# Performance work log

Measured on AMD Instinct MI355X. Metric: run time of the kernel, lower is better.

## Reference

```python
import jax, jax.numpy as jnp
import numpy as np

N, E = 50000, 800000
NFEAT, NHID, NCLASS = 512, 256, 64
RRELU_SLOPE = (1.0 / 8.0 + 1.0 / 3.0) / 2.0  # nn.RReLU eval-mode negative slope


def spmm(row, col, val, X):
    # sparse adj (COO: row, col, val) @ dense X -> [N, F]
    return jax.ops.segment_sum(X[col] * val[:, None], row, num_segments=N)


def setup_inputs() -> dict:
    key = jax.random.key(0)
    ks = jax.random.split(key, 12)
    x = jax.random.normal(ks[0], (N, NFEAT), dtype=jnp.float32)
    edge_row = jnp.sort(jax.random.randint(ks[1], (E,), 0, N))
    edge_col = jax.random.randint(ks[2], (E,), 0, N)
    # normalized-ish positive adjacency values
    edge_val = jax.random.uniform(ks[3], (E,), dtype=jnp.float32) / 16.0
    def glorot(k, fi, fo):
        s = 1.0 / np.sqrt(fi)
        return jax.random.normal(k, (fi, fo), dtype=jnp.float32) * s
    w1 = glorot(ks[4], NFEAT, NHID)
    b1 = jax.random.normal(ks[5], (NHID,), dtype=jnp.float32) * 0.01
    w2 = glorot(ks[6], NFEAT, NHID)
    b2 = jax.random.normal(ks[7], (NHID,), dtype=jnp.float32) * 0.01
    w3 = glorot(ks[8], NHID, NCLASS)
    b3 = jax.random.normal(ks[9], (NCLASS,), dtype=jnp.float32) * 0.01
    w4 = glorot(ks[10], NFEAT, NCLASS)
    b4 = jax.random.normal(ks[11], (NCLASS,), dtype=jnp.float32) * 0.01
    return {"x": x, "edge_row": edge_row, "edge_col": edge_col, "edge_val": edge_val,
            "w1": w1, "b1": b1, "w2": w2, "b2": b2, "w3": w3, "b3": b3, "w4": w4, "b4": b4}


def reference(x, edge_row, edge_col, edge_val, w1, b1, w2, b2, w3, b3, w4, b4):
    # skip branches (no adj): support = x @ W + b; dropout is identity in eval
    a_skip0 = x @ w2 + b2                                   # [N, NHID]
    a_skip1 = x @ w4 + b4                                   # [N, NCLASS]
    # gc1 with adj
    h1 = spmm(edge_row, edge_col, edge_val, x @ w1) + b1    # [N, NHID]
    v = h1 + a_skip0
    h = jnp.where(v >= 0, v, v * RRELU_SLOPE)               # RReLU (eval mode)
    # gc3 with adj
    out = spmm(edge_row, edge_col, edge_val, h @ w3) + b3 + a_skip1  # [N, NCLASS]
    return (out, w1, w2, w3, w4)
```

## Files before the change

kernel.cpp:

```cpp
#include <hip/hip_runtime.h>

#define N_NODES 50000
#define N_EDGES 800000
#define NFEAT 512
#define NHID 256
#define NCLASS 64
#define NCOMB 576
#define NPAD 640
#define NSKIP 320
#define RRELU_SLOPE 0.2291666666666667f

typedef __attribute__((ext_vector_type(8))) short bf16x8;
typedef __attribute__((ext_vector_type(4))) float f32x4;
typedef __attribute__((ext_vector_type(2))) float f32x2;

#define GLOAD_LDS16(g, l)                                                      \
    __builtin_amdgcn_global_load_lds(                                          \
        (const __attribute__((address_space(1))) void*)(g),                    \
        (__attribute__((address_space(3))) void*)(l), 16, 0, 0)

__device__ __forceinline__ unsigned short f2bf(float f) {
    unsigned int x = __float_as_uint(f);
    unsigned int r = (x + 0x7fffu + ((x >> 16) & 1u)) >> 16;
    return (unsigned short)r;
}
__device__ __forceinline__ float bf2f(unsigned short u) {
    return __uint_as_float(((unsigned int)u) << 16);
}
__device__ __forceinline__ float bf_lo(unsigned int u) { return __uint_as_float(u << 16); }
__device__ __forceinline__ float bf_hi(unsigned int u) { return __uint_as_float(u & 0xffff0000u); }
__device__ __forceinline__ unsigned char f2fp8(float v) {
    return (unsigned char)__builtin_amdgcn_cvt_pk_fp8_f32(v, v, 0, false);
}

#define S0 6400000
#define S1 6727680
#define S2 6728320
#define PREP_BLOCKS ((S2 + 255) / 256)

__global__ __launch_bounds__(256)
void prep(const float* __restrict__ x, const float* __restrict__ w1,
          const float* __restrict__ w2, const float* __restrict__ w4,
          const float* __restrict__ b1, const float* __restrict__ b2,
          const float* __restrict__ b3, const float* __restrict__ b4,
          unsigned short* __restrict__ xb, unsigned short* __restrict__ Bt,
          float* __restrict__ biasb) {
    int i = blockIdx.x * 256 + threadIdx.x;
    if (i >= S2) return;
    if (i < S0) {
        float4 v = ((const float4*)x)[i];
        ushort4 o;
        o.x = f2bf(v.x); o.y = f2bf(v.y); o.z = f2bf(v.z); o.w = f2bf(v.w);
        ((ushort4*)xb)[i] = o;
    } else if (i < S1) {
        int j = i - S0;
        int c = j >> 9;
        int k = j & 511;
        float v = 0.f;
        if (c < NHID)            v = w1[k * NHID + c];
        else if (c < 2 * NHID)   v = w2[k * NHID + (c - NHID)];
        else if (c < NCOMB)      v = w4[k * NCLASS + (c - 2 * NHID)];
        Bt[j] = f2bf(v);
    } else {
        int b = i - S1;
        float v = 0.f;
        if (b >= NHID && b < 2 * NHID)       v = b1[b - NHID] + b2[b - NHID];
        else if (b >= 2 * NHID && b < NCOMB) v = b3[b - 2 * NHID] + b4[b - 2 * NHID];
        biasb[b] = v;
    }
}

#define GBM 128
#define GBK 64
#define NCB0 5
#define NRP0 392
#define T0 800000
#define T1 850001
#define T2 866385
#define T3 944209
#define TAIL_BLOCKS ((T3 + 255) / 256)

template <int BN, int MODE>
__global__ __launch_bounds__(256, 4)
void gemm_bf16(const unsigned short* __restrict__ A,
               const unsigned short* __restrict__ Bt,
               const float* __restrict__ bias,
               unsigned char* __restrict__ C8,
               unsigned short* __restrict__ skipb,
               int M, int K, int NC,
               const int* __restrict__ erow, const int* __restrict__ ecol,
               const float* __restrict__ ev, const float* __restrict__ w1f,
               const float* __restrict__ w2f, const float* __restrict__ w3f,
               const float* __restrict__ w4f, uint2* __restrict__ ep,
               int* __restrict__ rp, unsigned short* __restrict__ w3t,
               float* __restrict__ outw) {
    constexpr int CF = BN / 32;
    __shared__ unsigned short As[GBM * GBK];
    __shared__ unsigned short Bs[BN * GBK];
    int row0, col0;
    if (MODE == 0) {
        int b = blockIdx.x;
        if (b >= NRP0 * NCB0) {
            int i = (b - NRP0 * NCB0) * 256 + threadIdx.x;
            if (i < T0) {
                uint2 e;
                e.x = (unsigned)ecol[i];
                e.y = __float_as_uint(ev[i]);
                ep[i] = e;
            } else if (i < T1) {
                int n = i - T0;
                int lo = 0, hi = N_EDGES;
                while (lo < hi) {
                    int mid = (lo + hi) >> 1;
                    if (erow[mid] < n) lo = mid + 1; else hi = mid;
                }
                rp[n] = lo;
            } else if (i < T2) {
                int j = i - T1;
                int c = j >> 8;
                int k = j & 255;
                w3t[j] = f2bf(w3f[k * NCLASS + c]);
            } else if (i < T3) {
                int j = i - T2;
                float4* o4 = (float4*)outw;
                if (j < 32768)        o4[800000 + j] = ((const float4*)w1f)[j];
                else if (j < 65536)   o4[832768 + (j - 32768)] = ((const float4*)w2f)[j - 32768];
                else if (j < 69632)   o4[865536 + (j - 65536)] = ((const float4*)w3f)[j - 65536];
                else                  o4[869632 + (j - 69632)] = ((const float4*)w4f)[j - 69632];
            }
            return;
        }
        int g = b / (8 * NCB0);
        int w = b % (8 * NCB0);
        int r = g * 8 + (w & 7);
        int c = w >> 3;
        if (r * GBM >= M) return;
        row0 = r * GBM;
        col0 = c * BN;
    } else {
        col0 = blockIdx.x * BN;
        row0 = blockIdx.y * GBM;
    }
    const int tid  = threadIdx.x;
    const int lane = tid & 63;
    const int wave = tid >> 6;
    const int wr = (wave >> 1) * 64;
    const int wc = (wave & 1) * (BN / 2);
    const int lm = lane & 15;
    const int l4 = lane >> 4;
    const int sw = lm & 7;

    const int sub  = lane >> 3;
    const int slot = lane & 7;
    const int goct = slot ^ sub;

    f32x4 acc[4][CF] = {};

    for (int k0 = 0; k0 < K; k0 += GBK) {
        #pragma unroll
        for (int p = 0; p < 4; ++p) {
            int chunk = wave * 4 + p;
            int gr = row0 + chunk * 8 + sub;
            if (gr > M - 1) gr = M - 1;
            GLOAD_LDS16(A + (size_t)gr * K + k0 + goct * 8, As + chunk * 512);
        }
        #pragma unroll
        for (int p = 0; p < BN / 32; ++p) {
            int chunk = wave * (BN / 32) + p;
            int rb = col0 + chunk * 8 + sub;
            GLOAD_LDS16(Bt + (size_t)rb * K + k0 + goct * 8, Bs + chunk * 512);
        }
        __syncthreads();

        #pragma unroll
        for (int kk8 = 0; kk8 < GBK / 8; kk8 += 4) {
            const int so = ((kk8 + l4) ^ sw) * 8;
            bf16x8 bfr[CF];
            #pragma unroll
            for (int j = 0; j < CF; ++j)
                bfr[j] = *(const bf16x8*)(Bs + (wc + j * 16 + lm) * 64 + so);
            #pragma unroll
            for (int i = 0; i < 4; ++i) {
                bf16x8 af = *(const bf16x8*)(As + (wr + i * 16 + lm) * 64 + so);
                #pragma unroll
                for (int j = 0; j < CF; ++j)
                    acc[i][j] = __builtin_amdgcn_mfma_f32_16x16x32_bf16(af, bfr[j], acc[i][j], 0, 0, 0);
            }
        }
        __syncthreads();
    }

    #pragma unroll
    for (int i = 0; i < 4; ++i) {
        #pragma unroll
        for (int j = 0; j < CF; ++j) {
            int col = col0 + wc + j * 16 + lm;
            float bvv = (MODE == 0) ? bias[col] : 0.f;
            #pragma unroll
            for (int r = 0; r < 4; ++r) {
                int row = row0 + wr + i * 16 + l4 * 4 + r;
                if (row < M) {
                    float v = acc[i][j][r];
                    if (MODE == 0) {
                        if (col < NHID)       C8[(size_t)row * NHID + col] = f2fp8(v);
                        else if (col < NCOMB) skipb[(size_t)row * NSKIP + (col - NHID)] = f2bf(v + bvv);
                    } else {
                        C8[(size_t)row * NC + col] = f2fp8(v);
                    }
                }
            }
        }
    }
}

__global__ __launch_bounds__(256)
void spmm1_rrelu(const int* __restrict__ rp, const uint2* __restrict__ ep,
                 const unsigned char* __restrict__ xw1q,
                 const unsigned short* __restrict__ skipb,
                 unsigned short* __restrict__ hb, int n_nodes) {
    int n = blockIdx.x * 8 + (threadIdx.x >> 5);
    if (n >= n_nodes) return;
    int l = threadIdx.x & 31;
    int f = l * 8;
    int lo = rp[n], hi = rp[n + 1];
    float s0 = 0.f, s1 = 0.f, s2 = 0.f, s3 = 0.f;
    float s4 = 0.f, s5 = 0.f, s6 = 0.f, s7 = 0.f;
    for (int e = lo; e < hi; e += 8) {
        uint2 ed[8];
        uint2 p[8];
        #pragma unroll
        for (int q = 0; q < 8; ++q) {
            int idx = (e + q < hi) ? e + q : hi - 1;
            ed[q] = ep[idx];
        }
        #pragma unroll
        for (int q = 0; q < 8; ++q)
            p[q] = *(const uint2*)(xw1q + (size_t)ed[q].x * NHID + f);
        #pragma unroll
        for (int q = 0; q < 8; ++q) {
            float v = (e + q < hi) ? __uint_as_float(ed[q].y) : 0.f;
            f32x2 ab = __builtin_amdgcn_cvt_pk_f32_fp8((int)p[q].x, false);
            f32x2 cd = __builtin_amdgcn_cvt_pk_f32_fp8((int)p[q].x, true);
            f32x2 ef = __builtin_amdgcn_cvt_pk_f32_fp8((int)p[q].y, false);
            f32x2 gh = __builtin_amdgcn_cvt_pk_f32_fp8((int)p[q].y, true);
            s0 += v * ab.x; s1 += v * ab.y;
            s2 += v * cd.x; s3 += v * cd.y;
            s4 += v * ef.x; s5 += v * ef.y;
            s6 += v * gh.x; s7 += v * gh.y;
        }
    }
    uint4 sk = *(const uint4*)(skipb + (size_t)n * NSKIP + f);
    float v0 = s0 + bf_lo(sk.x), v1 = s1 + bf_hi(sk.x);
    float v2 = s2 + bf_lo(sk.y), v3 = s3 + bf_hi(sk.y);
    float v4 = s4 + bf_lo(sk.z), v5 = s5 + bf_hi(sk.z);
    float v6 = s6 + bf_lo(sk.w), v7 = s7 + bf_hi(sk.w);
    v0 = (v0 >= 0.f) ? v0 : v0 * RRELU_SLOPE;
    v1 = (v1 >= 0.f) ? v1 : v1 * RRELU_SLOPE;
    v2 = (v2 >= 0.f) ? v2 : v2 * RRELU_SLOPE;
    v3 = (v3 >= 0.f) ? v3 : v3 * RRELU_SLOPE;
    v4 = (v4 >= 0.f) ? v4 : v4 * RRELU_SLOPE;
    v5 = (v5 >= 0.f) ? v5 : v5 * RRELU_SLOPE;
    v6 = (v6 >= 0.f) ? v6 : v6 * RRELU_SLOPE;
    v7 = (v7 >= 0.f) ? v7 : v7 * RRELU_SLOPE;
    uint4 o;
    o.x = (unsigned)f2bf(v0) | ((unsigned)f2bf(v1) << 16);
    o.y = (unsigned)f2bf(v2) | ((unsigned)f2bf(v3) << 16);
    o.z = (unsigned)f2bf(v4) | ((unsigned)f2bf(v5) << 16);
    o.w = (unsigned)f2bf(v6) | ((unsigned)f2bf(v7) << 16);
    *(uint4*)(hb + (size_t)n * NHID + f) = o;
}

__global__ __launch_bounds__(256)
void spmm2_out(const int* __restrict__ rp, const uint2* __restrict__ ep,
               const unsigned char* __restrict__ hw3q,
               const unsigned short* __restrict__ skipb,
               float* __restrict__ out, int n_nodes) {
    int n = blockIdx.x * 4 + (threadIdx.x >> 6);
    if (n >= n_nodes) return;
    int lane = threadIdx.x & 63;
    int q = lane >> 4;
    int l = lane & 15;
    int f = l * 4;
    int lo = rp[n], hi = rp[n + 1];
    float s0 = 0.f, s1 = 0.f, s2 = 0.f, s3 = 0.f;
    for (int e = lo + q; e < hi; e += 8) {
        int i1 = (e + 4 < hi) ? e + 4 : hi - 1;
        uint2 ea = ep[e], eb = ep[i1];
        unsigned pa = *(const unsigned*)(hw3q + (size_t)ea.x * NCLASS + f);
        unsigned pb = *(const unsigned*)(hw3q + (size_t)eb.x * NCLASS + f);
        float va = __uint_as_float(ea.y);
        float vb = (e + 4 < hi) ? __uint_as_float(eb.y) : 0.f;
        f32x2 a0 = __builtin_amdgcn_cvt_pk_f32_fp8((int)pa, false);
        f32x2 a1 = __builtin_amdgcn_cvt_pk_f32_fp8((int)pa, true);
        f32x2 b0 = __builtin_amdgcn_cvt_pk_f32_fp8((int)pb, false);
        f32x2 b1 = __builtin_amdgcn_cvt_pk_f32_fp8((int)pb, true);
        s0 += va * a0.x + vb * b0.x;
        s1 += va * a0.y + vb * b0.y;
        s2 += va * a1.x + vb * b1.x;
        s3 += va * a1.y + vb * b1.y;
    }
    s0 += __shfl_xor(s0, 16); s0 += __shfl_xor(s0, 32);
    s1 += __shfl_xor(s1, 16); s1 += __shfl_xor(s1, 32);
    s2 += __shfl_xor(s2, 16); s2 += __shfl_xor(s2, 32);
    s3 += __shfl_xor(s3, 16); s3 += __shfl_xor(s3, 32);
    if (q == 0) {
        uint2 sv = *(const uint2*)(skipb + (size_t)n * NSKIP + NHID + f);
        float4 o;
        o.x = s0 + bf_lo(sv.x);
        o.y = s1 + bf_hi(sv.x);
        o.z = s2 + bf_lo(sv.y);
        o.w = s3 + bf_hi(sv.y);
        *(float4*)(out + (size_t)n * NCLASS + f) = o;
    }
}

extern "C" void kernel_launch(void* const* d_in, const int* in_sizes, int n_in,
                              void* d_out, int out_size, void* d_ws, size_t ws_size,
                              hipStream_t stream) {
    const float* x    = (const float*)d_in[0];
    const int*   erow = (const int*)d_in[1];
    const int*   ecol = (const int*)d_in[2];
    const float* ev   = (const float*)d_in[3];
    const float* w1   = (const float*)d_in[4];
    const float* b1   = (const float*)d_in[5];
    const float* w2   = (const float*)d_in[6];
    const float* b2   = (const float*)d_in[7];
    const float* w3   = (const float*)d_in[8];
    const float* b3   = (const float*)d_in[9];
    const float* w4   = (const float*)d_in[10];
    const float* b4   = (const float*)d_in[11];
    float* out = (float*)d_out;

    char* ws = (char*)d_ws;
    size_t off = 0;
    auto alloc = [&](size_t bytes) -> void* {
        off = (off + 255) & ~(size_t)255;
        void* p = ws + off;
        off += bytes;
        return p;
    };

    unsigned short* xb    = (unsigned short*)alloc((size_t)N_NODES * NFEAT * 2);
    unsigned short* Bt    = (unsigned short*)alloc((size_t)NFEAT * NPAD * 2);
    float*          biasb = (float*)alloc(NPAD * 4);
    unsigned char*  xw1q  = (unsigned char*)alloc((size_t)N_NODES * NHID);
    unsigned short* skipb = (unsigned short*)alloc((size_t)N_NODES * NSKIP * 2);
    unsigned short* hb    = (unsigned short*)alloc((size_t)N_NODES * NHID * 2);
    unsigned short* w3t   = (unsigned short*)alloc((size_t)NHID * NCLASS * 2);
    unsigned char*  hw3q  = (unsigned char*)alloc((size_t)N_NODES * NCLASS);
    int*            rp    = (int*)alloc((size_t)(N_NODES + 1) * 4);
    uint2*          ep    = (uint2*)alloc((size_t)N_EDGES * 8);

    prep<<<PREP_BLOCKS, 256, 0, stream>>>(x, w1, w2, w4, b1, b2, b3, b4,
                                          xb, Bt, biasb);

    gemm_bf16<128, 0><<<NRP0 * NCB0 + TAIL_BLOCKS, 256, 0, stream>>>(
        xb, Bt, biasb, xw1q, skipb, N_NODES, NFEAT, NPAD,
        erow, ecol, ev, w1, w2, w3, w4, ep, rp, w3t, out);

    spmm1_rrelu<<<(N_NODES + 7) / 8, 256, 0, stream>>>(rp, ep, xw1q, skipb, hb, N_NODES);

    dim3 g2(NCLASS / 64, (N_NODES + GBM - 1) / GBM);
    gemm_bf16<64, 1><<<g2, 256, 0, stream>>>(hb, w3t, nullptr, hw3q, nullptr,
                                             N_NODES, NHID, NCLASS,
                                             nullptr, nullptr, nullptr, nullptr,
                                             nullptr, nullptr, nullptr, nullptr,
                                             nullptr, nullptr, nullptr);

    spmm2_out<<<(N_NODES + 3) / 4, 256, 0, stream>>>(rp, ep, hw3q, skipb, out, N_NODES);
}
```

Measured before the change: 299.5 us.

## Double-buffer GEMM LDS tiles, grid-stride prep, and narrower spmm2 node groups

The bf16 GEMM now uses 32-wide K tiles in two LDS buffers. The next tile is prefetched while the current one is being computed, so each iteration has a single barrier, and a matching XOR swizzle is applied. The prep kernel splits weight/bias packing from the x conversion, which now runs as a grid-stride loop over a fixed block count. spmm2 assigns 32 lanes per node with 8 fp8 features per lane, putting more nodes in each block. Smaller K tiles double the loop iterations, and with no wait before the next compute the correctness of the async loads depends on the single barrier ordering.

```diff
diff --git a/kernel.cpp b/kernel.cpp
--- a/kernel.cpp
+++ b/kernel.cpp
@@ -33,10 +33,11 @@
     return (unsigned char)__builtin_amdgcn_cvt_pk_fp8_f32(v, v, 0, false);
 }
 
-#define S0 6400000
-#define S1 6727680
-#define S2 6728320
-#define PREP_BLOCKS ((S2 + 255) / 256)
+#define P_BT 327680
+#define P_TOT 328320
+#define PK_BLK 1283
+#define XC_BLK 2048
+#define XC_N 6400000
 
 __global__ __launch_bounds__(256)
 void prep(const float* __restrict__ x, const float* __restrict__ w1,
@@ -45,33 +46,36 @@
           const float* __restrict__ b3, const float* __restrict__ b4,
           unsigned short* __restrict__ xb, unsigned short* __restrict__ Bt,
           float* __restrict__ biasb) {
-    int i = blockIdx.x * 256 + threadIdx.x;
-    if (i >= S2) return;
-    if (i < S0) {
+    int b = blockIdx.x;
+    if (b < PK_BLK) {
+        int i = b * 256 + threadIdx.x;
+        if (i < P_BT) {
+            int c = i >> 9;
+            int k = i & 511;
+            float v = 0.f;
+            if (c < NHID)            v = w1[k * NHID + c];
+            else if (c < 2 * NHID)   v = w2[k * NHID + (c - NHID)];
+            else if (c < NCOMB)      v = w4[k * NCLASS + (c - 2 * NHID)];
+            Bt[i] = f2bf(v);
+        } else if (i < P_TOT) {
+            int bb = i - P_BT;
+            float v = 0.f;
+            if (bb >= NHID && bb < 2 * NHID)       v = b1[bb - NHID] + b2[bb - NHID];
+            else if (bb >= 2 * NHID && bb < NCOMB) v = b3[bb - 2 * NHID] + b4[bb - 2 * NHID];
+            biasb[bb] = v;
+        }
+        return;
+    }
+    for (int i = (b - PK_BLK) * 256 + threadIdx.x; i < XC_N; i += XC_BLK * 256) {
         float4 v = ((const float4*)x)[i];
         ushort4 o;
         o.x = f2bf(v.x); o.y = f2bf(v.y); o.z = f2bf(v.z); o.w = f2bf(v.w);
         ((ushort4*)xb)[i] = o;
-    } else if (i < S1) {
-        int j = i - S0;
-        int c = j >> 9;
-        int k = j & 511;
-        float v = 0.f;
-        if (c < NHID)            v = w1[k * NHID + c];
-        else if (c < 2 * NHID)   v = w2[k * NHID + (c - NHID)];
-        else if (c < NCOMB)      v = w4[k * NCLASS + (c - 2 * NHID)];
-        Bt[j] = f2bf(v);
-    } else {
-        int b = i - S1;
-        float v = 0.f;
-        if (b >= NHID && b < 2 * NHID)       v = b1[b - NHID] + b2[b - NHID];
-        else if (b >= 2 * NHID && b < NCOMB) v = b3[b - 2 * NHID] + b4[b - 2 * NHID];
-        biasb[b] = v;
     }
 }
 
 #define GBM 128
-#define GBK 64
+#define GBK 32
 #define NCB0 5
 #define NRP0 392
 #define T0 800000
@@ -95,8 +99,8 @@
                int* __restrict__ rp, unsigned short* __restrict__ w3t,
                float* __restrict__ outw) {
     constexpr int CF = BN / 32;
-    __shared__ unsigned short As[GBM * GBK];
-    __shared__ unsigned short Bs[BN * GBK];
+    __shared__ unsigned short As[2 * GBM * GBK];
+    __shared__ unsigned short Bs[2 * BN * GBK];
     int row0, col0;
     if (MODE == 0) {
         int b = blockIdx.x;
@@ -148,46 +152,55 @@
     const int wc = (wave & 1) * (BN / 2);
     const int lm = lane & 15;
     const int l4 = lane >> 4;
-    const int sw = lm & 7;
-
-    const int sub  = lane >> 3;
-    const int slot = lane & 7;
-    const int goct = slot ^ sub;
+    const int kb = (lm >> 1) & 3;
+
+    const int sub16 = lane >> 2;
+    const int gs4   = (lane & 3) ^ ((sub16 >> 1) & 3);
 
     f32x4 acc[4][CF] = {};
 
-    for (int k0 = 0; k0 < K; k0 += GBK) {
-        #pragma unroll
-        for (int p = 0; p < 4; ++p) {
-            int chunk = wave * 4 + p;
-            int gr = row0 + chunk * 8 + sub;
+    auto stage = [&](int k0, int bf) {
+        #pragma unroll
+        for (int p = 0; p < 2; ++p) {
+            int c = wave * 2 + p;
+            int gr = row0 + c * 16 + sub16;
             if (gr > M - 1) gr = M - 1;
-            GLOAD_LDS16(A + (size_t)gr * K + k0 + goct * 8, As + chunk * 512);
-        }
-        #pragma unroll
-        for (int p = 0; p < BN / 32; ++p) {
-            int chunk = wave * (BN / 32) + p;
-            int rb = col0 + chunk * 8 + sub;
-            GLOAD_LDS16(Bt + (size_t)rb * K + k0 + goct * 8, Bs + chunk * 512);
-        }
-        __syncthreads();
-
-        #pragma unroll
-        for (int kk8 = 0; kk8 < GBK / 8; kk8 += 4) {
-            const int so = ((kk8 + l4) ^ sw) * 8;
-            bf16x8 bfr[CF];
+            GLOAD_LDS16(A + (size_t)gr * K + k0 + gs4 * 8,
+                        As + bf * (GBM * GBK) + c * 512);
+        }
+        #pragma unroll
+        for (int p = 0; p < BN / 64; ++p) {
+            int c = wave * (BN / 64) + p;
+            int rb = col0 + c * 16 + sub16;
+            GLOAD_LDS16(Bt + (size_t)rb * K + k0 + gs4 * 8,
+                        Bs + bf * (BN * GBK) + c * 512);
+        }
+    };
+
+    stage(0, 0);
+    __syncthreads();
+
+    const int nt = K / GBK;
+    int cur = 0;
+    for (int t = 0; t < nt; ++t) {
+        if (t + 1 < nt) stage((t + 1) * GBK, cur ^ 1);
+
+        const unsigned short* Ab = As + cur * (GBM * GBK);
+        const unsigned short* Bb = Bs + cur * (BN * GBK);
+        bf16x8 bfr[CF];
+        #pragma unroll
+        for (int j = 0; j < CF; ++j)
+            bfr[j] = *(const bf16x8*)(Bb + (wc + j * 16 + lm) * 32 + ((l4 ^ kb) * 8));
+        #pragma unroll
+        for (int i = 0; i < 4; ++i) {
+            bf16x8 af = *(const bf16x8*)(Ab + (wr + i * 16 + lm) * 32 + ((l4 ^ kb) * 8));
             #pragma unroll
             for (int j = 0; j < CF; ++j)
-                bfr[j] = *(const bf16x8*)(Bs + (wc + j * 16 + lm) * 64 + so);
-            #pragma unroll
-            for (int i = 0; i < 4; ++i) {
-                bf16x8 af = *(const bf16x8*)(As + (wr + i * 16 + lm) * 64 + so);
-                #pragma unroll
-                for (int j = 0; j < CF; ++j)
-                    acc[i][j] = __builtin_amdgcn_mfma_f32_16x16x32_bf16(af, bfr[j], acc[i][j], 0, 0, 0);
-            }
-        }
+                acc[i][j] = __builtin_amdgcn_mfma_f32_16x16x32_bf16(af, bfr[j], acc[i][j], 0, 0, 0);
+        }
+
         __syncthreads();
+        cur ^= 1;
     }
 
     #pragma unroll
@@ -275,42 +288,56 @@
                const unsigned char* __restrict__ hw3q,
                const unsigned short* __restrict__ skipb,
                float* __restrict__ out, int n_nodes) {
-    int n = blockIdx.x * 4 + (threadIdx.x >> 6);
+    int n = blockIdx.x * 8 + (threadIdx.x >> 5);
     if (n >= n_nodes) return;
-    int lane = threadIdx.x & 63;
-    int q = lane >> 4;
-    int l = lane & 15;
-    int f = l * 4;
+    int l = threadIdx.x & 31;
+    int oct = l >> 3;
+    int f = (l & 7) * 8;
     int lo = rp[n], hi = rp[n + 1];
     float s0 = 0.f, s1 = 0.f, s2 = 0.f, s3 = 0.f;
-    for (int e = lo + q; e < hi; e += 8) {
+    float s4 = 0.f, s5 = 0.f, s6 = 0.f, s7 = 0.f;
+    for (int e = lo + oct; e < hi; e += 8) {
         int i1 = (e + 4 < hi) ? e + 4 : hi - 1;
         uint2 ea = ep[e], eb = ep[i1];
-        unsigned pa = *(const unsigned*)(hw3q + (size_t)ea.x * NCLASS + f);
-        unsigned pb = *(const unsigned*)(hw3q + (size_t)eb.x * NCLASS + f);
+        uint2 pa = *(const uint2*)(hw3q + (size_t)ea.x * NCLASS + f);
+        uint2 pb = *(const uint2*)(hw3q + (size_t)eb.x * NCLASS + f);
         float va = __uint_as_float(ea.y);
         float vb = (e + 4 < hi) ? __uint_as_float(eb.y) : 0.f;
-        f32x2 a0 = __builtin_amdgcn_cvt_pk_f32_fp8((int)pa, false);
-        f32x2 a1 = __builtin_amdgcn_cvt_pk_f32_fp8((int)pa, true);
-        f32x2 b0 = __builtin_amdgcn_cvt_pk_f32_fp8((int)pb, false);
-        f32x2 b1 = __builtin_amdgcn_cvt_pk_f32_fp8((int)pb, true);
+        f32x2 a0 = __builtin_amdgcn_cvt_pk_f32_fp8((int)pa.x, false);
+        f32x2 a1 = __builtin_amdgcn_cvt_pk_f32_fp8((int)pa.x, true);
+        f32x2 a2 = __builtin_amdgcn_cvt_pk_f32_fp8((int)pa.y, false);
+        f32x2 a3 = __builtin_amdgcn_cvt_pk_f32_fp8((int)pa.y, true);
+        f32x2 b0 = __builtin_amdgcn_cvt_pk_f32_fp8((int)pb.x, false);
+        f32x2 b1 = __builtin_amdgcn_cvt_pk_f32_fp8((int)pb.x, true);
+        f32x2 b2 = __builtin_amdgcn_cvt_pk_f32_fp8((int)pb.y, false);
+        f32x2 b3 = __builtin_amdgcn_cvt_pk_f32_fp8((int)pb.y, true);
         s0 += va * a0.x + vb * b0.x;
         s1 += va * a0.y + vb * b0.y;
         s2 += va * a1.x + vb * b1.x;
         s3 += va * a1.y + vb * b1.y;
-    }
-    s0 += __shfl_xor(s0, 16); s0 += __shfl_xor(s0, 32);
-    s1 += __shfl_xor(s1, 16); s1 += __shfl_xor(s1, 32);
-    s2 += __shfl_xor(s2, 16); s2 += __shfl_xor(s2, 32);
-    s3 += __shfl_xor(s3, 16); s3 += __shfl_xor(s3, 32);
-    if (q == 0) {
-        uint2 sv = *(const uint2*)(skipb + (size_t)n * NSKIP + NHID + f);
-        float4 o;
-        o.x = s0 + bf_lo(sv.x);
-        o.y = s1 + bf_hi(sv.x);
-        o.z = s2 + bf_lo(sv.y);
-        o.w = s3 + bf_hi(sv.y);
-        *(float4*)(out + (size_t)n * NCLASS + f) = o;
+        s4 += va * a2.x + vb * b2.x;
+        s5 += va * a2.y + vb * b2.y;
+        s6 += va * a3.x + vb * b3.x;
+        s7 += va * a3.y + vb * b3.y;
+    }
+    s0 += __shfl_xor(s0, 8); s0 += __shfl_xor(s0, 16);
+    s1 += __shfl_xor(s1, 8); s1 += __shfl_xor(s1, 16);
+    s2 += __shfl_xor(s2, 8); s2 += __shfl_xor(s2, 16);
+    s3 += __shfl_xor(s3, 8); s3 += __shfl_xor(s3, 16);
+    s4 += __shfl_xor(s4, 8); s4 += __shfl_xor(s4, 16);
+    s5 += __shfl_xor(s5, 8); s5 += __shfl_xor(s5, 16);
+    s6 += __shfl_xor(s6, 8); s6 += __shfl_xor(s6, 16);
+    s7 += __shfl_xor(s7, 8); s7 += __shfl_xor(s7, 16);
+    if (oct == 0) {
+        uint4 sv = *(const uint4*)(skipb + (size_t)n * NSKIP + NHID + f);
+        float4 o1, o2;
+        o1.x = s0 + bf_lo(sv.x); o1.y = s1 + bf_hi(sv.x);
+        o1.z = s2 + bf_lo(sv.y); o1.w = s3 + bf_hi(sv.y);
+        o2.x = s4 + bf_lo(sv.z); o2.y = s5 + bf_hi(sv.z);
+        o2.z = s6 + bf_lo(sv.w); o2.w = s7 + bf_hi(sv.w);
+        float4* op = (float4*)(out + (size_t)n * NCLASS + f);
+        op[0] = o1;
+        op[1] = o2;
     }
 }
 
@@ -351,8 +378,8 @@
     int*            rp    = (int*)alloc((size_t)(N_NODES + 1) * 4);
     uint2*          ep    = (uint2*)alloc((size_t)N_EDGES * 8);
 
-    prep<<<PREP_BLOCKS, 256, 0, stream>>>(x, w1, w2, w4, b1, b2, b3, b4,
-                                          xb, Bt, biasb);
+    prep<<<PK_BLK + XC_BLK, 256, 0, stream>>>(x, w1, w2, w4, b1, b2, b3, b4,
+                                              xb, Bt, biasb);
 
     gemm_bf16<128, 0><<<NRP0 * NCB0 + TAIL_BLOCKS, 256, 0, stream>>>(
         xb, Bt, biasb, xw1q, skipb, N_NODES, NFEAT, NPAD,
@@ -367,5 +394,5 @@
                                              nullptr, nullptr, nullptr, nullptr,
                                              nullptr, nullptr, nullptr);
 
-    spmm2_out<<<(N_NODES + 3) / 4, 256, 0, stream>>>(rp, ep, hw3q, skipb, out, N_NODES);
-}
+    spmm2_out<<<(N_NODES + 7) / 8, 256, 0, stream>>>(rp, ep, hw3q, skipb, out, N_NODES);
+}
```

After: 305.7 us. 1.02x slower.
